# Kernel tuning notes

Hardware: AMD Instinct MI355X
Metric: run time of the kernel (lower is better)

Reference implementation:

```python
import jax, jax.numpy as jnp
import numpy as np

TEMPERATURE = 0.5
EPS = 1e-8  # torch CosineSimilarity eps


def setup_inputs() -> dict:
    key = jax.random.key(0)
    k1, k2 = jax.random.split(key)
    B, D = 4096, 256
    return {
        "z_i": jax.random.normal(k1, (B, D), dtype=jnp.float32),
        "z_j": jax.random.normal(k2, (B, D), dtype=jnp.float32),
    }


def reference(z_i, z_j):
    B = z_i.shape[0]
    N = 2 * B
    z = jnp.concatenate([z_i, z_j], axis=0)  # [N, D]
    # cosine similarity == normalized dot product (eps-clamped norms like torch)
    norms = jnp.maximum(jnp.linalg.norm(z, axis=1, keepdims=True), EPS)
    zn = z / norms
    sim = jnp.matmul(zn, zn.T) / TEMPERATURE  # [N, N]

    idx = jnp.arange(B)
    # positives: diag(sim, +B) and diag(sim, -B)
    pos = jnp.concatenate([sim[idx, idx + B], sim[idx + B, idx]])  # [N]

    # CrossEntropy with label 0 over [pos_i, negatives_i] reduces to
    # logsumexp over row i excluding the self-diagonal, minus pos_i.
    r = jnp.arange(N)
    neg_inf = jnp.finfo(sim.dtype).min
    sim_masked = jnp.where(r[:, None] == r[None, :], neg_inf, sim)
    lse = jax.nn.logsumexp(sim_masked, axis=1)  # [N]

    loss = (jnp.sum(lse) - jnp.sum(pos)) / N
    return loss
```

## Files before the change

### kernel.cpp

```cpp
#include <hip/hip_runtime.h>
#include <cstdint>

#define B_ROWS 4096
#define N_ROWS 8192
#define D_DIM  256
#define BT     128
#define TGRID  64
#define NTILES 2080
#define BK     32
#define NKT    8

typedef __attribute__((ext_vector_type(4))) float f32x4;
typedef __attribute__((ext_vector_type(8))) short bf16x8;
typedef __attribute__((ext_vector_type(4))) unsigned short u16x4;

__device__ __forceinline__ unsigned short f2bf(float f) {
    union { float f; unsigned u; } v; v.f = f;
    unsigned r = v.u + 0x7FFF + ((v.u >> 16) & 1);
    return (unsigned short)(r >> 16);
}
__device__ __forceinline__ float bf2f(unsigned short h) {
    union { unsigned u; float f; } v; v.u = ((unsigned)h) << 16;
    return v.f;
}

__device__ __forceinline__ void gload16(const void* g, void* l) {
    __builtin_amdgcn_global_load_lds(
        (const __attribute__((address_space(1))) void*)g,
        (__attribute__((address_space(3))) void*)l, 16, 0, 0);
}

__device__ __forceinline__ f32x4 exp4(f32x4 v) {
    f32x4 r;
    r.x = __expf(v.x); r.y = __expf(v.y); r.z = __expf(v.z); r.w = __expf(v.w);
    return r;
}

__global__ __launch_bounds__(256) void normpos_kernel(const float* __restrict__ zi,
                                                      const float* __restrict__ zj,
                                                      unsigned short* __restrict__ zn,
                                                      float* __restrict__ pospartial) {
    int wid = threadIdx.x >> 6;
    int lane = threadIdx.x & 63;
    int p = blockIdx.x * 4 + wid;
    f32x4 ga = *(const f32x4*)(zi + (size_t)p * D_DIM + lane * 4);
    f32x4 gb = *(const f32x4*)(zj + (size_t)p * D_DIM + lane * 4);
    float sa = ga.x * ga.x + ga.y * ga.y + ga.z * ga.z + ga.w * ga.w;
    float sb = gb.x * gb.x + gb.y * gb.y + gb.z * gb.z + gb.w * gb.w;
    #pragma unroll
    for (int m = 1; m < 64; m <<= 1) { sa += __shfl_xor(sa, m, 64); sb += __shfl_xor(sb, m, 64); }
    float fa = 1.41421356237309515f / fmaxf(sqrtf(sa), 1e-8f);
    float fb = 1.41421356237309515f / fmaxf(sqrtf(sb), 1e-8f);
    u16x4 oa, ob;
    oa.x = f2bf(ga.x * fa); oa.y = f2bf(ga.y * fa); oa.z = f2bf(ga.z * fa); oa.w = f2bf(ga.w * fa);
    ob.x = f2bf(gb.x * fb); ob.y = f2bf(gb.y * fb); ob.z = f2bf(gb.z * fb); ob.w = f2bf(gb.w * fb);
    *(u16x4*)(zn + (size_t)p * D_DIM + lane * 4) = oa;
    *(u16x4*)(zn + (size_t)(p + B_ROWS) * D_DIM + lane * 4) = ob;
    float d = bf2f(oa.x) * bf2f(ob.x) + bf2f(oa.y) * bf2f(ob.y)
            + bf2f(oa.z) * bf2f(ob.z) + bf2f(oa.w) * bf2f(ob.w);
    #pragma unroll
    for (int m = 1; m < 64; m <<= 1) d += __shfl_xor(d, m, 64);
    if (lane == 0) pospartial[p] = d;
}

__global__ __launch_bounds__(256, 3) void simclr_gemm_kernel(const unsigned short* __restrict__ zn,
                                                             float* __restrict__ P) {
    __shared__ unsigned short As[BT * BK];
    __shared__ unsigned short Bs[BT * BK];
    __shared__ float rPpart[2][BT];
    __shared__ float cPpart[2][BT];

    const int tid = threadIdx.x;
    const int lane = tid & 63, wid = tid >> 6;
    const int wr = wid >> 1, wc = wid & 1;

    int bid = (int)((blockIdx.x & 7) * (NTILES / 8) + (blockIdx.x >> 3));
    int ti = (int)((129.0f - sqrtf(16641.0f - 8.0f * (float)bid)) * 0.5f);
    while ((ti + 1) * TGRID - ((ti + 1) * ti) / 2 <= bid) ++ti;
    while (ti * TGRID - (ti * (ti - 1)) / 2 > bid) --ti;
    const int tj = ti + (bid - (ti * TGRID - (ti * (ti - 1)) / 2));

    const char* gA = (const char*)zn + (size_t)ti * BT * 512;
    const char* gB = (const char*)zn + (size_t)tj * BT * 512;

    const int r0 = tid >> 2;
    const int sch = (tid & 3) ^ ((tid >> 3) & 3);
    const size_t gof0 = (size_t)r0 * 512 + (size_t)sch * 16;
    const size_t gof1 = (size_t)(64 + r0) * 512 + (size_t)sch * 16;
    const unsigned lo0 = (unsigned)tid * 8;
    const unsigned lo1 = 2048u + (unsigned)tid * 8;

    f32x4 acc[4][4];
    #pragma unroll
    for (int m = 0; m < 4; ++m)
        #pragma unroll
        for (int n = 0; n < 4; ++n)
            acc[m][n] = (f32x4){0.f, 0.f, 0.f, 0.f};

    const int kc = (lane >> 4) ^ (((lane & 15) >> 1) & 3);
    const int arow = wr * 64 + (lane & 15);
    const int brow = wc * 64 + (lane & 15);

    #pragma unroll
    for (int kt = 0; kt < NKT; ++kt) {
        const size_t kb = (size_t)kt * 64;
        gload16(gA + gof0 + kb, &As[lo0]);
        gload16(gA + gof1 + kb, &As[lo1]);
        gload16(gB + gof0 + kb, &Bs[lo0]);
        gload16(gB + gof1 + kb, &Bs[lo1]);
        __syncthreads();

        bf16x8 af[4], bfr[4];
        #pragma unroll
        for (int m = 0; m < 4; ++m)
            af[m] = *(const bf16x8*)&As[(arow + m * 16) * 32 + kc * 8];
        #pragma unroll
        for (int n = 0; n < 4; ++n)
            bfr[n] = *(const bf16x8*)&Bs[(brow + n * 16) * 32 + kc * 8];

        #pragma unroll
        for (int m = 0; m < 4; ++m)
            #pragma unroll
            for (int n = 0; n < 4; ++n)
                acc[m][n] = __builtin_amdgcn_mfma_f32_16x16x32_bf16(af[m], bfr[n], acc[m][n], 0, 0, 0);
        __syncthreads();
    }

    float cs[4] = {0.f, 0.f, 0.f, 0.f};
    #pragma unroll
    for (int m = 0; m < 4; ++m) {
        f32x4 ef[4];
        #pragma unroll
        for (int n = 0; n < 4; ++n) ef[n] = exp4(acc[m][n]);
        f32x4 rv = ef[0] + ef[1] + ef[2] + ef[3];
        #pragma unroll
        for (int msk = 1; msk <= 8; msk <<= 1) {
            rv.x += __shfl_xor(rv.x, msk, 64);
            rv.y += __shfl_xor(rv.y, msk, 64);
            rv.z += __shfl_xor(rv.z, msk, 64);
            rv.w += __shfl_xor(rv.w, msk, 64);
        }
        if ((lane & 15) == 0) {
            int rbase = wr * 64 + m * 16 + (lane >> 4) * 4;
            rPpart[wc][rbase + 0] = rv.x;
            rPpart[wc][rbase + 1] = rv.y;
            rPpart[wc][rbase + 2] = rv.z;
            rPpart[wc][rbase + 3] = rv.w;
        }
        #pragma unroll
        for (int n = 0; n < 4; ++n)
            cs[n] += ef[n].x + ef[n].y + ef[n].z + ef[n].w;
    }
    #pragma unroll
    for (int n = 0; n < 4; ++n) {
        float c = cs[n];
        c += __shfl_xor(c, 16, 64);
        c += __shfl_xor(c, 32, 64);
        if (lane < 16) cPpart[wr][wc * 64 + n * 16 + lane] = c;
    }
    __syncthreads();

    if (tid < BT) {
        P[(size_t)tj * N_ROWS + ti * BT + tid] = rPpart[0][tid] + rPpart[1][tid];
    } else if (ti != tj) {
        int t = tid - BT;
        P[(size_t)ti * N_ROWS + tj * BT + t] = cPpart[0][t] + cPpart[1][t];
    }
}

__global__ __launch_bounds__(256) void reduce_rows_kernel(const float* __restrict__ P,
                                                          const float* __restrict__ pospartial,
                                                          float* __restrict__ blockpart) {
    const float E2 = 7.38905609893065f;
    int row = blockIdx.x * 256 + threadIdx.x;
    float s = 0.f;
    #pragma unroll 16
    for (int src = 0; src < TGRID; ++src)
        s += P[(size_t)src * N_ROWS + row];
    float v = logf(s - E2);
    if (threadIdx.x < 128)
        v -= 2.0f * pospartial[blockIdx.x * 128 + threadIdx.x];
    #pragma unroll
    for (int m = 1; m < 64; m <<= 1) v += __shfl_xor(v, m, 64);
    __shared__ float ws[4];
    if ((threadIdx.x & 63) == 0) ws[threadIdx.x >> 6] = v;
    __syncthreads();
    if (threadIdx.x == 0) blockpart[blockIdx.x] = ws[0] + ws[1] + ws[2] + ws[3];
}

__global__ __launch_bounds__(64) void final_kernel(const float* __restrict__ blockpart,
                                                   float* __restrict__ out) {
    int lane = threadIdx.x;
    float v = (lane < 32) ? blockpart[lane] : 0.f;
    #pragma unroll
    for (int m = 1; m < 64; m <<= 1) v += __shfl_xor(v, m, 64);
    if (lane == 0) out[0] = v / (float)N_ROWS;
}

extern "C" void kernel_launch(void* const* d_in, const int* in_sizes, int n_in,
                              void* d_out, int out_size, void* d_ws, size_t ws_size,
                              hipStream_t stream) {
    const float* zi = (const float*)d_in[0];
    const float* zj = (const float*)d_in[1];
    char* ws = (char*)d_ws;
    unsigned short* zn = (unsigned short*)ws;
    float* P = (float*)(ws + 4 * 1024 * 1024);
    float* pospartial = (float*)(ws + 6 * 1024 * 1024);
    float* blockpart = (float*)(ws + 6 * 1024 * 1024 + 16 * 1024);

    normpos_kernel<<<B_ROWS / 4, 256, 0, stream>>>(zi, zj, zn, pospartial);
    simclr_gemm_kernel<<<NTILES, 256, 0, stream>>>(zn, P);
    reduce_rows_kernel<<<N_ROWS / 256, 256, 0, stream>>>(P, pospartial, blockpart);
    final_kernel<<<1, 64, 0, stream>>>(blockpart, (float*)d_out);
}
```

Measured before the change: 45.29 us.

## Keep A panel in registers and sweep four column tiles per block

Each block now loads its 128-row A panel once into registers (32 bf16x8 fragments per lane) and processes up to four consecutive upper-triangular column tiles. B tiles stream through a double-buffered LDS stage, with the next load issued before the current MFMAs. The grid shrinks from 2080 to 544 blocks. This cuts redundant A traffic and per-block launch and prologue overhead, at the cost of much higher register pressure (occupancy hint lowered to 2), more LDS, and possible load imbalance because the triangle rows leave some blocks with fewer tiles.

Result: slower. 69.91 us (+54.4%).

```diff
diff --git a/kernel.cpp b/kernel.cpp
--- a/kernel.cpp
+++ b/kernel.cpp
@@ -6,8 +6,8 @@
 #define D_DIM  256
 #define BT     128
 #define TGRID  64
-#define NTILES 2080
-#define BK     32
+#define NJ     4
+#define NBLOCKS 544
 #define NKT    8
 
 typedef __attribute__((ext_vector_type(4))) float f32x4;
@@ -63,10 +63,10 @@
     if (lane == 0) pospartial[p] = d;
 }
 
-__global__ __launch_bounds__(256, 3) void simclr_gemm_kernel(const unsigned short* __restrict__ zn,
+__global__ __launch_bounds__(256, 2) void simclr_gemm_kernel(const unsigned short* __restrict__ zn,
                                                              float* __restrict__ P) {
-    __shared__ unsigned short As[BT * BK];
-    __shared__ unsigned short Bs[BT * BK];
+    __shared__ unsigned short Astage[4 * 4096];
+    __shared__ unsigned short Bs[2][4096];
     __shared__ float rPpart[2][BT];
     __shared__ float cPpart[2][BT];
 
@@ -74,14 +74,19 @@
     const int lane = tid & 63, wid = tid >> 6;
     const int wr = wid >> 1, wc = wid & 1;
 
-    int bid = (int)((blockIdx.x & 7) * (NTILES / 8) + (blockIdx.x >> 3));
-    int ti = (int)((129.0f - sqrtf(16641.0f - 8.0f * (float)bid)) * 0.5f);
-    while ((ti + 1) * TGRID - ((ti + 1) * ti) / 2 <= bid) ++ti;
-    while (ti * TGRID - (ti * (ti - 1)) / 2 > bid) --ti;
-    const int tj = ti + (bid - (ti * TGRID - (ti * (ti - 1)) / 2));
+    int bid = (int)((blockIdx.x & 7) * (NBLOCKS / 8) + (blockIdx.x >> 3));
+    int ti = 0, cum = 0;
+    for (;;) {
+        int c = (TGRID - ti + 3) >> 2;
+        if (bid < cum + c) break;
+        cum += c; ++ti;
+    }
+    const int jc = bid - cum;
+    const int j0 = ti + 4 * jc;
+    const int nj = min(NJ, TGRID - j0);
+    const int G = nj * NKT;
 
     const char* gA = (const char*)zn + (size_t)ti * BT * 512;
-    const char* gB = (const char*)zn + (size_t)tj * BT * 512;
 
     const int r0 = tid >> 2;
     const int sch = (tid & 3) ^ ((tid >> 3) & 3);
@@ -90,82 +95,108 @@
     const unsigned lo0 = (unsigned)tid * 8;
     const unsigned lo1 = 2048u + (unsigned)tid * 8;
 
-    f32x4 acc[4][4];
-    #pragma unroll
-    for (int m = 0; m < 4; ++m)
-        #pragma unroll
-        for (int n = 0; n < 4; ++n)
-            acc[m][n] = (f32x4){0.f, 0.f, 0.f, 0.f};
-
     const int kc = (lane >> 4) ^ (((lane & 15) >> 1) & 3);
     const int arow = wr * 64 + (lane & 15);
     const int brow = wc * 64 + (lane & 15);
 
-    #pragma unroll
-    for (int kt = 0; kt < NKT; ++kt) {
-        const size_t kb = (size_t)kt * 64;
-        gload16(gA + gof0 + kb, &As[lo0]);
-        gload16(gA + gof1 + kb, &As[lo1]);
-        gload16(gB + gof0 + kb, &Bs[lo0]);
-        gload16(gB + gof1 + kb, &Bs[lo1]);
+    bf16x8 af[4][8];
+    #pragma unroll
+    for (int h = 0; h < 2; ++h) {
+        #pragma unroll
+        for (int s = 0; s < 4; ++s) {
+            size_t kb = (size_t)(h * 4 + s) * 64;
+            gload16(gA + gof0 + kb, &Astage[s * 4096 + lo0]);
+            gload16(gA + gof1 + kb, &Astage[s * 4096 + lo1]);
+        }
         __syncthreads();
-
-        bf16x8 af[4], bfr[4];
-        #pragma unroll
-        for (int m = 0; m < 4; ++m)
-            af[m] = *(const bf16x8*)&As[(arow + m * 16) * 32 + kc * 8];
-        #pragma unroll
-        for (int n = 0; n < 4; ++n)
-            bfr[n] = *(const bf16x8*)&Bs[(brow + n * 16) * 32 + kc * 8];
-
-        #pragma unroll
-        for (int m = 0; m < 4; ++m)
-            #pragma unroll
-            for (int n = 0; n < 4; ++n)
-                acc[m][n] = __builtin_amdgcn_mfma_f32_16x16x32_bf16(af[m], bfr[n], acc[m][n], 0, 0, 0);
+        #pragma unroll
+        for (int s = 0; s < 4; ++s)
+            #pragma unroll
+            for (int m = 0; m < 4; ++m)
+                af[m][h * 4 + s] = *(const bf16x8*)&Astage[s * 4096 + (arow + m * 16) * 32 + kc * 8];
         __syncthreads();
     }
 
-    float cs[4] = {0.f, 0.f, 0.f, 0.f};
-    #pragma unroll
-    for (int m = 0; m < 4; ++m) {
-        f32x4 ef[4];
-        #pragma unroll
-        for (int n = 0; n < 4; ++n) ef[n] = exp4(acc[m][n]);
-        f32x4 rv = ef[0] + ef[1] + ef[2] + ef[3];
-        #pragma unroll
-        for (int msk = 1; msk <= 8; msk <<= 1) {
-            rv.x += __shfl_xor(rv.x, msk, 64);
-            rv.y += __shfl_xor(rv.y, msk, 64);
-            rv.z += __shfl_xor(rv.z, msk, 64);
-            rv.w += __shfl_xor(rv.w, msk, 64);
-        }
-        if ((lane & 15) == 0) {
-            int rbase = wr * 64 + m * 16 + (lane >> 4) * 4;
-            rPpart[wc][rbase + 0] = rv.x;
-            rPpart[wc][rbase + 1] = rv.y;
-            rPpart[wc][rbase + 2] = rv.z;
-            rPpart[wc][rbase + 3] = rv.w;
-        }
+#define STAGE_B(g_) do {                                                     \
+    int jt_ = (g_) >> 3;                                                     \
+    size_t kb_ = (size_t)((g_) & 7) * 64;                                    \
+    const char* gBp = (const char*)zn + (size_t)(j0 + jt_) * BT * 512;       \
+    gload16(gBp + gof0 + kb_, &Bs[(g_) & 1][lo0]);                           \
+    gload16(gBp + gof1 + kb_, &Bs[(g_) & 1][lo1]);                           \
+} while (0)
+
+    STAGE_B(0);
+
+    f32x4 acc[4][4];
+    #pragma unroll
+    for (int m = 0; m < 4; ++m)
         #pragma unroll
         for (int n = 0; n < 4; ++n)
-            cs[n] += ef[n].x + ef[n].y + ef[n].z + ef[n].w;
+            acc[m][n] = (f32x4){0.f, 0.f, 0.f, 0.f};
+
+    for (int jt = 0; jt < nj; ++jt) {
+        const int tj = j0 + jt;
+        #pragma unroll
+        for (int kt = 0; kt < NKT; ++kt) {
+            const int g = jt * NKT + kt;
+            __syncthreads();
+            bf16x8 bfr[4];
+            #pragma unroll
+            for (int n = 0; n < 4; ++n)
+                bfr[n] = *(const bf16x8*)&Bs[g & 1][(brow + n * 16) * 32 + kc * 8];
+            if (g + 1 < G) STAGE_B(g + 1);
+            #pragma unroll
+            for (int m = 0; m < 4; ++m)
+                #pragma unroll
+                for (int n = 0; n < 4; ++n)
+                    acc[m][n] = __builtin_amdgcn_mfma_f32_16x16x32_bf16(af[m][kt], bfr[n], acc[m][n], 0, 0, 0);
+        }
+
+        float cs[4] = {0.f, 0.f, 0.f, 0.f};
+        #pragma unroll
+        for (int m = 0; m < 4; ++m) {
+            f32x4 ef[4];
+            #pragma unroll
+            for (int n = 0; n < 4; ++n) ef[n] = exp4(acc[m][n]);
+            #pragma unroll
+            for (int n = 0; n < 4; ++n)
+                acc[m][n] = (f32x4){0.f, 0.f, 0.f, 0.f};
+            f32x4 rv = ef[0] + ef[1] + ef[2] + ef[3];
+            #pragma unroll
+            for (int msk = 1; msk <= 8; msk <<= 1) {
+                rv.x += __shfl_xor(rv.x, msk, 64);
+                rv.y += __shfl_xor(rv.y, msk, 64);
+                rv.z += __shfl_xor(rv.z, msk, 64);
+                rv.w += __shfl_xor(rv.w, msk, 64);
+            }
+            if ((lane & 15) == 0) {
+                int rbase = wr * 64 + m * 16 + (lane >> 4) * 4;
+                rPpart[wc][rbase + 0] = rv.x;
+                rPpart[wc][rbase + 1] = rv.y;
+                rPpart[wc][rbase + 2] = rv.z;
+                rPpart[wc][rbase + 3] = rv.w;
+            }
+            #pragma unroll
+            for (int n = 0; n < 4; ++n)
+                cs[n] += ef[n].x + ef[n].y + ef[n].z + ef[n].w;
+        }
+        #pragma unroll
+        for (int n = 0; n < 4; ++n) {
+            float c = cs[n];
+            c += __shfl_xor(c, 16, 64);
+            c += __shfl_xor(c, 32, 64);
+            if (lane < 16) cPpart[wr][wc * 64 + n * 16 + lane] = c;
+        }
+        __syncthreads();
+
+        if (tid < BT) {
+            P[(size_t)tj * N_ROWS + (size_t)ti * BT + tid] = rPpart[0][tid] + rPpart[1][tid];
+        } else if (tj != ti) {
+            int t = tid - BT;
+            P[(size_t)ti * N_ROWS + (size_t)tj * BT + t] = cPpart[0][t] + cPpart[1][t];
+        }
     }
-    #pragma unroll
-    for (int n = 0; n < 4; ++n) {
-        float c = cs[n];
-        c += __shfl_xor(c, 16, 64);
-        c += __shfl_xor(c, 32, 64);
-        if (lane < 16) cPpart[wr][wc * 64 + n * 16 + lane] = c;
-    }
-    __syncthreads();
-
-    if (tid < BT) {
-        P[(size_t)tj * N_ROWS + ti * BT + tid] = rPpart[0][tid] + rPpart[1][tid];
-    } else if (ti != tj) {
-        int t = tid - BT;
-        P[(size_t)ti * N_ROWS + tj * BT + t] = cPpart[0][t] + cPpart[1][t];
-    }
+#undef STAGE_B
 }
 
 __global__ __launch_bounds__(256) void reduce_rows_kernel(const float* __restrict__ P,
@@ -209,7 +240,7 @@
     float* blockpart = (float*)(ws + 6 * 1024 * 1024 + 16 * 1024);
 
     normpos_kernel<<<B_ROWS / 4, 256, 0, stream>>>(zi, zj, zn, pospartial);
-    simclr_gemm_kernel<<<NTILES, 256, 0, stream>>>(zn, P);
+    simclr_gemm_kernel<<<NBLOCKS, 256, 0, stream>>>(zn, P);
     reduce_rows_kernel<<<N_ROWS / 256, 256, 0, stream>>>(P, pospartial, blockpart);
     final_kernel<<<1, 64, 0, stream>>>(blockpart, (float*)d_out);
 }
```

## Quantize normalized embeddings to FP8 e4m3 and use FP8 MFMA for similarity GEMM

Applied to the files above, without the earlier changes.

Normalized rows are now encoded as FP8 e4m3 with a software converter and stored in a byte layout permuted to match the MFMA operand order. The GEMM runs fp8 16x16x32 MFMAs with half as many K-tiles, and the positive-pair dot product is computed in full FP32. This halves the bytes staged through LDS and global memory and uses the higher-rate FP8 matrix path. In exchange, the similarity logits lose precision, which may shift the loss beyond tolerance.

Result: faster. 38.24 us (median of 2 runs) (-15.6%).

```diff
diff --git a/kernel.cpp b/kernel.cpp
--- a/kernel.cpp
+++ b/kernel.cpp
@@ -7,22 +7,10 @@
 #define BT     128
 #define TGRID  64
 #define NTILES 2080
-#define BK     32
-#define NKT    8
+#define NKT    4
 
 typedef __attribute__((ext_vector_type(4))) float f32x4;
-typedef __attribute__((ext_vector_type(8))) short bf16x8;
-typedef __attribute__((ext_vector_type(4))) unsigned short u16x4;
-
-__device__ __forceinline__ unsigned short f2bf(float f) {
-    union { float f; unsigned u; } v; v.f = f;
-    unsigned r = v.u + 0x7FFF + ((v.u >> 16) & 1);
-    return (unsigned short)(r >> 16);
-}
-__device__ __forceinline__ float bf2f(unsigned short h) {
-    union { unsigned u; float f; } v; v.u = ((unsigned)h) << 16;
-    return v.f;
-}
+typedef __attribute__((ext_vector_type(2))) unsigned long u64x2;
 
 __device__ __forceinline__ void gload16(const void* g, void* l) {
     __builtin_amdgcn_global_load_lds(
@@ -36,9 +24,26 @@
     return r;
 }
 
+__device__ __forceinline__ unsigned f2e4m3(float f) {
+    union { float f; unsigned u; } v; v.f = f;
+    unsigned s = (v.u >> 24) & 0x80u;
+    unsigned mag = v.u & 0x7fffffffu;
+    int e = (int)(mag >> 23) - 127;
+    if (e >= -6) {
+        unsigned r = mag + 0x7ffffu + ((mag >> 20) & 1u);
+        int e2 = (int)(r >> 23) - 127;
+        unsigned m3 = (r >> 20) & 7u;
+        return s | (unsigned)((e2 + 7) << 3) | m3;
+    }
+    if (e < -10) return s;
+    float q = rintf(fabsf(f) * 512.0f);
+    unsigned qi = (unsigned)q;
+    return s | qi;
+}
+
 __global__ __launch_bounds__(256) void normpos_kernel(const float* __restrict__ zi,
                                                       const float* __restrict__ zj,
-                                                      unsigned short* __restrict__ zn,
+                                                      unsigned char* __restrict__ zn,
                                                       float* __restrict__ pospartial) {
     int wid = threadIdx.x >> 6;
     int lane = threadIdx.x & 63;
@@ -51,22 +56,24 @@
     for (int m = 1; m < 64; m <<= 1) { sa += __shfl_xor(sa, m, 64); sb += __shfl_xor(sb, m, 64); }
     float fa = 1.41421356237309515f / fmaxf(sqrtf(sa), 1e-8f);
     float fb = 1.41421356237309515f / fmaxf(sqrtf(sb), 1e-8f);
-    u16x4 oa, ob;
-    oa.x = f2bf(ga.x * fa); oa.y = f2bf(ga.y * fa); oa.z = f2bf(ga.z * fa); oa.w = f2bf(ga.w * fa);
-    ob.x = f2bf(gb.x * fb); ob.y = f2bf(gb.y * fb); ob.z = f2bf(gb.z * fb); ob.w = f2bf(gb.w * fb);
-    *(u16x4*)(zn + (size_t)p * D_DIM + lane * 4) = oa;
-    *(u16x4*)(zn + (size_t)(p + B_ROWS) * D_DIM + lane * 4) = ob;
-    float d = bf2f(oa.x) * bf2f(ob.x) + bf2f(oa.y) * bf2f(ob.y)
-            + bf2f(oa.z) * bf2f(ob.z) + bf2f(oa.w) * bf2f(ob.w);
+    f32x4 na, nb;
+    na.x = ga.x * fa; na.y = ga.y * fa; na.z = ga.z * fa; na.w = ga.w * fa;
+    nb.x = gb.x * fb; nb.y = gb.y * fb; nb.z = gb.z * fb; nb.w = gb.w * fb;
+    unsigned pa = f2e4m3(na.x) | (f2e4m3(na.y) << 8) | (f2e4m3(na.z) << 16) | (f2e4m3(na.w) << 24);
+    unsigned pb = f2e4m3(nb.x) | (f2e4m3(nb.y) << 8) | (f2e4m3(nb.z) << 16) | (f2e4m3(nb.w) << 24);
+    int bytepos = (lane >> 4) * 64 + ((lane >> 1) & 3) * 16 + ((lane >> 3) & 1) * 8 + 4 * (lane & 1);
+    *(unsigned*)(zn + (size_t)p * 256 + bytepos) = pa;
+    *(unsigned*)(zn + (size_t)(p + B_ROWS) * 256 + bytepos) = pb;
+    float d = na.x * nb.x + na.y * nb.y + na.z * nb.z + na.w * nb.w;
     #pragma unroll
     for (int m = 1; m < 64; m <<= 1) d += __shfl_xor(d, m, 64);
     if (lane == 0) pospartial[p] = d;
 }
 
-__global__ __launch_bounds__(256, 3) void simclr_gemm_kernel(const unsigned short* __restrict__ zn,
+__global__ __launch_bounds__(256, 3) void simclr_gemm_kernel(const unsigned char* __restrict__ zn,
                                                              float* __restrict__ P) {
-    __shared__ unsigned short As[BT * BK];
-    __shared__ unsigned short Bs[BT * BK];
+    __shared__ unsigned char As[BT * 64];
+    __shared__ unsigned char Bs[BT * 64];
     __shared__ float rPpart[2][BT];
     __shared__ float cPpart[2][BT];
 
@@ -80,15 +87,15 @@
     while (ti * TGRID - (ti * (ti - 1)) / 2 > bid) --ti;
     const int tj = ti + (bid - (ti * TGRID - (ti * (ti - 1)) / 2));
 
-    const char* gA = (const char*)zn + (size_t)ti * BT * 512;
-    const char* gB = (const char*)zn + (size_t)tj * BT * 512;
+    const char* gA = (const char*)zn + (size_t)ti * BT * 256;
+    const char* gB = (const char*)zn + (size_t)tj * BT * 256;
 
     const int r0 = tid >> 2;
     const int sch = (tid & 3) ^ ((tid >> 3) & 3);
-    const size_t gof0 = (size_t)r0 * 512 + (size_t)sch * 16;
-    const size_t gof1 = (size_t)(64 + r0) * 512 + (size_t)sch * 16;
-    const unsigned lo0 = (unsigned)tid * 8;
-    const unsigned lo1 = 2048u + (unsigned)tid * 8;
+    const size_t gof0 = (size_t)r0 * 256 + (size_t)sch * 16;
+    const size_t gof1 = (size_t)(64 + r0) * 256 + (size_t)sch * 16;
+    const unsigned lo0 = (unsigned)tid * 16;
+    const unsigned lo1 = 4096u + (unsigned)tid * 16;
 
     f32x4 acc[4][4];
     #pragma unroll
@@ -97,7 +104,7 @@
         for (int n = 0; n < 4; ++n)
             acc[m][n] = (f32x4){0.f, 0.f, 0.f, 0.f};
 
-    const int kc = (lane >> 4) ^ (((lane & 15) >> 1) & 3);
+    const int ysw = (lane >> 4) ^ (((lane & 15) >> 1) & 3);
     const int arow = wr * 64 + (lane & 15);
     const int brow = wc * 64 + (lane & 15);
 
@@ -110,19 +117,23 @@
         gload16(gB + gof1 + kb, &Bs[lo1]);
         __syncthreads();
 
-        bf16x8 af[4], bfr[4];
+        u64x2 af[4], bfr[4];
         #pragma unroll
         for (int m = 0; m < 4; ++m)
-            af[m] = *(const bf16x8*)&As[(arow + m * 16) * 32 + kc * 8];
+            af[m] = *(const u64x2*)&As[(arow + m * 16) * 64 + ysw * 16];
         #pragma unroll
         for (int n = 0; n < 4; ++n)
-            bfr[n] = *(const bf16x8*)&Bs[(brow + n * 16) * 32 + kc * 8];
+            bfr[n] = *(const u64x2*)&Bs[(brow + n * 16) * 64 + ysw * 16];
 
         #pragma unroll
         for (int m = 0; m < 4; ++m)
             #pragma unroll
-            for (int n = 0; n < 4; ++n)
-                acc[m][n] = __builtin_amdgcn_mfma_f32_16x16x32_bf16(af[m], bfr[n], acc[m][n], 0, 0, 0);
+            for (int n = 0; n < 4; ++n) {
+                acc[m][n] = __builtin_amdgcn_mfma_f32_16x16x32_fp8_fp8(
+                    (long)af[m].x, (long)bfr[n].x, acc[m][n], 0, 0, 0);
+                acc[m][n] = __builtin_amdgcn_mfma_f32_16x16x32_fp8_fp8(
+                    (long)af[m].y, (long)bfr[n].y, acc[m][n], 0, 0, 0);
+            }
         __syncthreads();
     }
 
@@ -203,10 +214,10 @@
     const float* zi = (const float*)d_in[0];
     const float* zj = (const float*)d_in[1];
     char* ws = (char*)d_ws;
-    unsigned short* zn = (unsigned short*)ws;
-    float* P = (float*)(ws + 4 * 1024 * 1024);
-    float* pospartial = (float*)(ws + 6 * 1024 * 1024);
-    float* blockpart = (float*)(ws + 6 * 1024 * 1024 + 16 * 1024);
+    unsigned char* zn = (unsigned char*)ws;
+    float* P = (float*)(ws + 2 * 1024 * 1024);
+    float* pospartial = (float*)(ws + 4 * 1024 * 1024);
+    float* blockpart = (float*)(ws + 4 * 1024 * 1024 + 16 * 1024);
 
     normpos_kernel<<<B_ROWS / 4, 256, 0, stream>>>(zi, zj, zn, pospartial);
     simclr_gemm_kernel<<<NTILES, 256, 0, stream>>>(zn, P);
```
